# Optimization experiments

Hardware: AMD Instinct MI355X
Metric: run time of the kernel (lower is better)

Reference implementation:

```python
import jax, jax.numpy as jnp
import numpy as np

E = 2048   # embed_dim
H = 16     # num query heads
D = E // H # head_dim = 128
B = 2
S = 2048


def setup_inputs() -> dict:
    key = jax.random.key(0)
    ks = jax.random.split(key, 12)
    sc = 0.02
    return {
        "input": jax.random.normal(ks[0], (B, S, E), jnp.float32),
        "kv": jax.random.normal(ks[1], (B, S, E), jnp.float32),
        "Wq": jax.random.normal(ks[2], (E, E), jnp.float32) * sc,
        "bq": jnp.zeros((E,), jnp.float32),
        "Wk": jax.random.normal(ks[3], (D, E), jnp.float32) * sc,
        "bk": jnp.zeros((D,), jnp.float32),
        "Wv": jax.random.normal(ks[4], (D, E), jnp.float32) * sc,
        "bv": jnp.zeros((D,), jnp.float32),
        "Wo": jax.random.normal(ks[5], (E, E), jnp.float32) * sc,
        "bo": jnp.zeros((E,), jnp.float32),
        "expanding_context": 0,
    }


def reference(input, kv, Wq, bq, Wk, bk, Wv, bv, Wo, bo, expanding_context):
    b, s, _ = input.shape
    # projections (torch Linear: x @ W.T + b)
    q = (input @ Wq.T + bq).reshape(b, s, H, D).transpose(0, 2, 1, 3)  # [B,H,S,D]
    k = kv @ Wk.T + bk  # [B,S,D] single KV head
    v = kv @ Wv.T + bv  # [B,S,D]
    # scores with single KV head broadcast across query heads
    scores = jnp.einsum('bhsd,btd->bhst', q, k) / jnp.sqrt(jnp.float32(D))
    causal = jnp.triu(jnp.ones((s, s), bool), k=1)  # True above diagonal
    scores = jnp.where(causal[None, None], jnp.float32(-jnp.inf), scores)
    attn = jax.nn.softmax(scores, axis=-1)
    out = jnp.einsum('bhst,btd->bhsd', attn, v)  # [B,H,S,D]
    out = out.transpose(0, 2, 1, 3).reshape(b, s, E)
    return out @ Wo.T + bo
```

## Files before the change

### kernel.cpp

```cpp
#include <hip/hip_runtime.h>

#define B_  2
#define S_  2048
#define E_  2048
#define H_  16
#define D_  128
#define BS_ (B_*S_)

typedef __bf16 bf16_t;
typedef __bf16 bf16x8 __attribute__((ext_vector_type(8)));
typedef __bf16 bf16x4 __attribute__((ext_vector_type(4)));
typedef float  f32x4  __attribute__((ext_vector_type(4)));
typedef float  f32x16 __attribute__((ext_vector_type(16)));

#define QSCALE 0.1275174131003543f

__device__ __forceinline__ void gld16(const bf16_t* g, bf16_t* l) {
    __builtin_amdgcn_global_load_lds(
        (const __attribute__((address_space(1))) void*)g,
        (__attribute__((address_space(3))) void*)l,
        16, 0, 0);
}

__global__ void cvt_all(const float* __restrict__ s0, const float* __restrict__ s1,
                        const float* __restrict__ s2, const float* __restrict__ s3,
                        const float* __restrict__ s4, const float* __restrict__ s5,
                        bf16_t* d0, bf16_t* d1, bf16_t* d2,
                        bf16_t* d3, bf16_t* d4, bf16_t* d5)
{
    long i = ((long)blockIdx.x * blockDim.x + threadIdx.x) * 4;
    const float* s; bf16_t* d;
    if      (i <  8388608) { s = s0; d = d0; }
    else if (i < 16777216) { s = s1; d = d1; i -=  8388608; }
    else if (i < 20971520) { s = s2; d = d2; i -= 16777216; }
    else if (i < 21233664) { s = s3; d = d3; i -= 20971520; }
    else if (i < 21495808) { s = s4; d = d4; i -= 21233664; }
    else                   { s = s5; d = d5; i -= 21495808; }
    float4 v = *(const float4*)(s + i);
    bf16x4 o;
    o[0] = (bf16_t)v.x; o[1] = (bf16_t)v.y; o[2] = (bf16_t)v.z; o[3] = (bf16_t)v.w;
    *(bf16x4*)(d + i) = o;
}

template<int EP>
__device__ __forceinline__ void gemm_tile128(
    const bf16_t* __restrict__ A, const bf16_t* __restrict__ W,
    const float* __restrict__ bias,
    float* __restrict__ Cf, bf16_t* __restrict__ Cb,
    int N, int K, float scale, int m0, int w_n0, int c_n0,
    bf16_t* As, bf16_t* Bs)
{
    const int tid  = threadIdx.x;
    const int wave = tid >> 6, lane = tid & 63;
    const int wm = wave >> 1, wn = wave & 1;
    const int lrow = lane & 15, quad = lane >> 4;
    const int r8 = lane >> 3, c8 = (lane & 7) << 3;

    f32x4 acc[4][4] = {};

    for (int k0 = 0; k0 < K; k0 += 64) {
        __syncthreads();
#pragma unroll
        for (int j = 0; j < 4; ++j) {
            int base = (wave * 4 + j) * 8;
            gld16(A + (size_t)(m0 + base + r8) * K + k0 + c8, &As[base * 64]);
        }
#pragma unroll
        for (int j = 0; j < 4; ++j) {
            int base = (wave * 4 + j) * 8;
            gld16(W + (size_t)(w_n0 + base + r8) * K + k0 + c8, &Bs[base * 64]);
        }
        __syncthreads();
#pragma unroll
        for (int ks = 0; ks < 2; ++ks) {
            bf16x8 af[4], bfr[4];
#pragma unroll
            for (int mt = 0; mt < 4; ++mt)
                af[mt] = *(const bf16x8*)&As[(wm * 64 + mt * 16 + lrow) * 64 + ks * 32 + quad * 8];
#pragma unroll
            for (int nt = 0; nt < 4; ++nt)
                bfr[nt] = *(const bf16x8*)&Bs[(wn * 64 + nt * 16 + lrow) * 64 + ks * 32 + quad * 8];
#pragma unroll
            for (int mt = 0; mt < 4; ++mt)
#pragma unroll
                for (int nt = 0; nt < 4; ++nt)
                    acc[mt][nt] = __builtin_amdgcn_mfma_f32_16x16x32_bf16(
                        af[mt], bfr[nt], acc[mt][nt], 0, 0, 0);
        }
    }

#pragma unroll
    for (int mt = 0; mt < 4; ++mt) {
#pragma unroll
        for (int nt = 0; nt < 4; ++nt) {
            int lcol = wn * 64 + nt * 16 + lrow;
            int col = c_n0 + lcol;
            float bvv = bias[lcol];
#pragma unroll
            for (int r = 0; r < 4; ++r) {
                int row = m0 + wm * 64 + mt * 16 + quad * 4 + r;
                float v = (acc[mt][nt][r] + bvv) * scale;
                if (EP == 0) Cf[(size_t)row * N + col] = v;
                else         Cb[(size_t)row * N + col] = (bf16_t)v;
            }
        }
    }
}

__global__ __launch_bounds__(256) void gemm_qkv(
    const bf16_t* __restrict__ xb, const bf16_t* __restrict__ kvb,
    const bf16_t* __restrict__ Wq, const bf16_t* __restrict__ Wkv,
    const float* __restrict__ bq, const float* __restrict__ bk,
    const float* __restrict__ bv,
    bf16_t* __restrict__ Qb, bf16_t* __restrict__ KVb)
{
    __shared__ __align__(16) bf16_t As[128 * 64];
    __shared__ __align__(16) bf16_t Bs[128 * 64];
    const int m0 = blockIdx.y * 128;
    const int x = blockIdx.x;
    if (x < 16) {
        int n0 = x * 128;
        gemm_tile128<1>(xb, Wq, bq + n0, nullptr, Qb, E_, E_, QSCALE,
                        m0, n0, n0, As, Bs);
    } else if (x == 16) {
        gemm_tile128<1>(kvb, Wkv, bk, nullptr, KVb, 256, E_, 1.0f,
                        m0, 0, 0, As, Bs);
    } else {
        gemm_tile128<1>(kvb, Wkv, bv, nullptr, KVb, 256, E_, 1.0f,
                        m0, 128, 128, As, Bs);
    }
}

__global__ __launch_bounds__(256) void gemm_o(
    const bf16_t* __restrict__ A, const bf16_t* __restrict__ W,
    const float* __restrict__ bias, float* __restrict__ Cf)
{
    __shared__ __align__(16) bf16_t As[128 * 64];
    __shared__ __align__(16) bf16_t Bs[128 * 64];
    int n0 = blockIdx.x * 128;
    gemm_tile128<0>(A, W, bias + n0, Cf, nullptr, E_, E_, 1.0f,
                    blockIdx.y * 128, n0, n0, As, Bs);
}

__global__ __launch_bounds__(256, 2) void mqa_attn(
    const bf16_t* __restrict__ Q, const bf16_t* __restrict__ KV,
    bf16_t* __restrict__ O)
{
    __shared__ __align__(16) bf16_t Kt[2][64][136];
    __shared__ __align__(16) bf16_t Vt[2][128][72];

    const int bx = blockIdx.x, h = blockIdx.y, b = blockIdx.z;
    const int qb = b ? bx : (15 - bx);
    const int tid = threadIdx.x, wave = tid >> 6, lane = tid & 63;
    const int ln = lane & 31, hi = lane >> 5;
    const int q0w = qb * 128 + wave * 32;

    const bf16_t* kvp = KV + (size_t)(b * S_) * 256;

    bf16x8 qf[8];
    {
        const bf16_t* qp = Q + ((size_t)(b * S_ + q0w + ln)) * E_ + h * D_ + hi * 8;
#pragma unroll
        for (int st = 0; st < 8; ++st) qf[st] = *(const bf16x8*)(qp + st * 16);
    }

    bf16x8 ones;
#pragma unroll
    for (int j = 0; j < 8; ++j) ones[j] = (bf16_t)1.0f;

    f32x16 oacc[4] = {};
    f32x16 racc = {};
    bf16x8 af[4] = {};

    const int NT = 2 * qb + 2;
    const int Tw = (q0w + 31) >> 6;

    bf16x8 kreg[4], vA[2], vB[2];
    auto loadKV = [&](int kt) {
        const int k0 = kt * 64;
#pragma unroll
        for (int i = 0; i < 4; ++i) {
            int c = tid + 256 * i;
            kreg[i] = *(const bf16x8*)(kvp + (size_t)(k0 + (c >> 4)) * 256 + ((c & 15) << 3));
        }
#pragma unroll
        for (int i = 0; i < 2; ++i) {
            int c = tid + 256 * i;
            int n = (c & 31) * 2, d0 = (c >> 5) << 3;
            const bf16_t* src = kvp + (size_t)(k0 + n) * 256 + 128 + d0;
            vA[i] = *(const bf16x8*)src;
            vB[i] = *(const bf16x8*)(src + 256);
        }
    };
    auto stageWrite = [&](int bb) {
#pragma unroll
        for (int i = 0; i < 4; ++i) {
            int c = tid + 256 * i;
            *(bf16x8*)&Kt[bb][c >> 4][(c & 15) << 3] = kreg[i];
        }
#pragma unroll
        for (int i = 0; i < 2; ++i) {
            int c = tid + 256 * i;
            int n = (c & 31) * 2, d0 = (c >> 5) << 3;
#pragma unroll
            for (int j = 0; j < 8; ++j) {
                union { bf16_t h[2]; unsigned u; } w2;
                w2.h[0] = vA[i][j]; w2.h[1] = vB[i][j];
                *(unsigned*)&Vt[bb][d0 + j][n] = w2.u;
            }
        }
    };
    auto doPV = [&](int vb) {
        __builtin_amdgcn_s_setprio(1);
#pragma unroll
        for (int ks = 0; ks < 4; ++ks)
#pragma unroll
            for (int dt = 0; dt < 4; ++dt) {
                bf16x8 vf = *(const bf16x8*)&Vt[vb][dt * 32 + ln][ks * 16 + hi * 8];
                oacc[dt] = __builtin_amdgcn_mfma_f32_32x32x16_bf16(af[ks], vf, oacc[dt], 0, 0, 0);
            }
        __builtin_amdgcn_s_setprio(0);
    };

    loadKV(0);
    stageWrite(0);
    if (NT > 1) loadKV(1);

    for (int t = 0; t < NT; ++t) {
        const int cur = t & 1;
        if (t >= 1 && t - 1 <= Tw) doPV(cur ^ 1);
        __syncthreads();
        if (t + 1 < NT) stageWrite(cur ^ 1);
        if (t + 2 < NT) loadKV(t + 2);
        if (t <= Tw) {
            f32x16 sc[2] = {f32x16{}, f32x16{}};
            __builtin_amdgcn_s_setprio(1);
#pragma unroll
            for (int st = 0; st < 8; ++st) {
                bf16x8 qv = qf[st];
#pragma unroll
                for (int ct = 0; ct < 2; ++ct) {
                    bf16x8 kf = *(const bf16x8*)&Kt[cur][ct * 32 + ln][st * 16 + hi * 8];
                    sc[ct] = __builtin_amdgcn_mfma_f32_32x32x16_bf16(kf, qv, sc[ct], 0, 0, 0);
                }
            }
            __builtin_amdgcn_s_setprio(0);
            const int k_base = t * 64;
            const int qi = q0w + ln;
            if (k_base + 63 > q0w) {
#pragma unroll
                for (int ct = 0; ct < 2; ++ct)
#pragma unroll
                    for (int r = 0; r < 16; ++r) {
                        int kj = k_base + ct * 32 + (r & 3) + 8 * (r >> 2) + 4 * hi;
                        float s = (kj > qi) ? -1e30f : sc[ct][r];
                        sc[ct][r] = exp2f(s);
                    }
            } else {
#pragma unroll
                for (int ct = 0; ct < 2; ++ct)
#pragma unroll
                    for (int r = 0; r < 16; ++r)
                        sc[ct][r] = exp2f(sc[ct][r]);
            }
#pragma unroll
            for (int ks = 0; ks < 4; ++ks) {
                const int c = ks >> 1, b8 = (ks & 1) * 8;
                union { bf16_t h[2]; unsigned u; } pk0, pk1, pk2, pk3;
                pk0.h[0] = (bf16_t)sc[c][b8 + 0]; pk0.h[1] = (bf16_t)sc[c][b8 + 1];
                pk1.h[0] = (bf16_t)sc[c][b8 + 2]; pk1.h[1] = (bf16_t)sc[c][b8 + 3];
                pk2.h[0] = (bf16_t)sc[c][b8 + 4]; pk2.h[1] = (bf16_t)sc[c][b8 + 5];
                pk3.h[0] = (bf16_t)sc[c][b8 + 6]; pk3.h[1] = (bf16_t)sc[c][b8 + 7];
                const unsigned U0 = pk0.u, U1 = pk1.u, U2 = pk2.u, U3 = pk3.u;
                const unsigned V0 = __shfl_xor(U0, 32);
                const unsigned V1 = __shfl_xor(U1, 32);
                const unsigned V2 = __shfl_xor(U2, 32);
                const unsigned V3 = __shfl_xor(U3, 32);
                union { unsigned u[4]; bf16x8 v; } W;
                W.u[0] = hi ? V2 : U0;
                W.u[1] = hi ? V3 : U1;
                W.u[2] = hi ? U2 : V0;
                W.u[3] = hi ? U3 : V1;
                af[ks] = W.v;
            }
#pragma unroll
            for (int ks = 0; ks < 4; ++ks)
                racc = __builtin_amdgcn_mfma_f32_32x32x16_bf16(af[ks], ones, racc, 0, 0, 0);
        }
    }
    if (Tw == NT - 1) doPV(1);

    float inv[16];
#pragma unroll
    for (int r = 0; r < 16; ++r) inv[r] = 1.0f / racc[r];
#pragma unroll
    for (int dt = 0; dt < 4; ++dt)
#pragma unroll
        for (int r = 0; r < 16; ++r) {
            int ro = (r & 3) + 8 * (r >> 2) + 4 * hi;
            O[((size_t)(b * S_ + q0w + ro)) * E_ + h * D_ + dt * 32 + ln] =
                (bf16_t)(oacc[dt][r] * inv[r]);
        }
}

extern "C" void kernel_launch(void* const* d_in, const int* in_sizes, int n_in,
                              void* d_out, int out_size, void* d_ws, size_t ws_size,
                              hipStream_t stream)
{
    const float* x   = (const float*)d_in[0];
    const float* kv  = (const float*)d_in[1];
    const float* Wq  = (const float*)d_in[2];
    const float* bq  = (const float*)d_in[3];
    const float* Wk  = (const float*)d_in[4];
    const float* bk  = (const float*)d_in[5];
    const float* Wv  = (const float*)d_in[6];
    const float* bv  = (const float*)d_in[7];
    const float* Wo  = (const float*)d_in[8];
    const float* bo  = (const float*)d_in[9];
    float* out = (float*)d_out;

    bf16_t* p    = (bf16_t*)d_ws;
    bf16_t* xb   = p;  p += (size_t)BS_ * E_;
    bf16_t* kvb  = p;  p += (size_t)BS_ * E_;
    bf16_t* Wqb  = p;  p += (size_t)E_ * E_;
    bf16_t* Wkvb = p;  p += (size_t)2 * D_ * E_;
    bf16_t* Wob  = p;  p += (size_t)E_ * E_;
    bf16_t* Qb   = p;  p += (size_t)BS_ * E_;
    bf16_t* KVb  = p;  p += (size_t)BS_ * 256;
    bf16_t* Ob   = p;  p += (size_t)BS_ * E_;

    cvt_all<<<dim3(25088), dim3(256), 0, stream>>>(
        x, kv, Wq, Wk, Wv, Wo,
        xb, kvb, Wqb, Wkvb, Wkvb + (size_t)D_ * E_, Wob);

    gemm_qkv<<<dim3(18, BS_ / 128), 256, 0, stream>>>(
        xb, kvb, Wqb, Wkvb, bq, bk, bv, Qb, KVb);

    mqa_attn<<<dim3(S_ / 128, H_, B_), 256, 0, stream>>>(Qb, KVb, Ob);

    gemm_o<<<dim3(E_ / 128, BS_ / 128), 256, 0, stream>>>(Ob, Wob, bo, out);
}
```

Measured before the change: 357.4 us.

## Split-K the Q and output projections in two, merging partials downstream

The Q projection and the output projection now split the K dimension into two halves via a z grid dimension. Each half writes a bf16 partial buffer. The two Q partials are summed, biased and scaled while the attention kernel loads Q, and a new merge kernel adds the output partials plus bias into the fp32 result. The aim is more blocks per GEMM for better CU utilisation, at the cost of extra partial-buffer traffic, an extra kernel launch and bf16 rounding of the partial sums.

```diff
diff --git a/kernel.cpp b/kernel.cpp
--- a/kernel.cpp
+++ b/kernel.cpp
@@ -46,8 +46,8 @@
 __device__ __forceinline__ void gemm_tile128(
     const bf16_t* __restrict__ A, const bf16_t* __restrict__ W,
     const float* __restrict__ bias,
-    float* __restrict__ Cf, bf16_t* __restrict__ Cb,
-    int N, int K, float scale, int m0, int w_n0, int c_n0,
+    bf16_t* __restrict__ Cb,
+    int N, int K, int kb, int ke, float scale, int m0, int w_n0, int c_n0,
     bf16_t* As, bf16_t* Bs)
 {
     const int tid  = threadIdx.x;
@@ -58,7 +58,7 @@
 
     f32x4 acc[4][4] = {};
 
-    for (int k0 = 0; k0 < K; k0 += 64) {
+    for (int k0 = kb; k0 < ke; k0 += 64) {
         __syncthreads();
 #pragma unroll
         for (int j = 0; j < 4; ++j) {
@@ -95,13 +95,13 @@
         for (int nt = 0; nt < 4; ++nt) {
             int lcol = wn * 64 + nt * 16 + lrow;
             int col = c_n0 + lcol;
-            float bvv = bias[lcol];
+            float bvv = (EP == 1) ? bias[lcol] : 0.f;
 #pragma unroll
             for (int r = 0; r < 4; ++r) {
                 int row = m0 + wm * 64 + mt * 16 + quad * 4 + r;
-                float v = (acc[mt][nt][r] + bvv) * scale;
-                if (EP == 0) Cf[(size_t)row * N + col] = v;
-                else         Cb[(size_t)row * N + col] = (bf16_t)v;
+                float v = (EP == 1) ? (acc[mt][nt][r] + bvv) * scale
+                                    : acc[mt][nt][r];
+                Cb[(size_t)row * N + col] = (bf16_t)v;
             }
         }
     }
@@ -110,41 +110,62 @@
 __global__ __launch_bounds__(256) void gemm_qkv(
     const bf16_t* __restrict__ xb, const bf16_t* __restrict__ kvb,
     const bf16_t* __restrict__ Wq, const bf16_t* __restrict__ Wkv,
-    const float* __restrict__ bq, const float* __restrict__ bk,
-    const float* __restrict__ bv,
-    bf16_t* __restrict__ Qb, bf16_t* __restrict__ KVb)
+    const float* __restrict__ bk, const float* __restrict__ bv,
+    bf16_t* __restrict__ Qp0, bf16_t* __restrict__ Qp1,
+    bf16_t* __restrict__ KVb)
 {
     __shared__ __align__(16) bf16_t As[128 * 64];
     __shared__ __align__(16) bf16_t Bs[128 * 64];
     const int m0 = blockIdx.y * 128;
-    const int x = blockIdx.x;
+    const int x = blockIdx.x, z = blockIdx.z;
     if (x < 16) {
         int n0 = x * 128;
-        gemm_tile128<1>(xb, Wq, bq + n0, nullptr, Qb, E_, E_, QSCALE,
-                        m0, n0, n0, As, Bs);
-    } else if (x == 16) {
-        gemm_tile128<1>(kvb, Wkv, bk, nullptr, KVb, 256, E_, 1.0f,
-                        m0, 0, 0, As, Bs);
-    } else {
-        gemm_tile128<1>(kvb, Wkv, bv, nullptr, KVb, 256, E_, 1.0f,
-                        m0, 128, 128, As, Bs);
+        bf16_t* Qz = z ? Qp1 : Qp0;
+        gemm_tile128<2>(xb, Wq, nullptr, Qz, E_, E_,
+                        z * 1024, z * 1024 + 1024, 1.0f, m0, n0, n0, As, Bs);
+    } else if (z == 0) {
+        if (x == 16)
+            gemm_tile128<1>(kvb, Wkv, bk, KVb, 256, E_, 0, E_, 1.0f,
+                            m0, 0, 0, As, Bs);
+        else
+            gemm_tile128<1>(kvb, Wkv, bv, KVb, 256, E_, 0, E_, 1.0f,
+                            m0, 128, 128, As, Bs);
     }
 }
 
 __global__ __launch_bounds__(256) void gemm_o(
     const bf16_t* __restrict__ A, const bf16_t* __restrict__ W,
-    const float* __restrict__ bias, float* __restrict__ Cf)
+    bf16_t* __restrict__ Op0, bf16_t* __restrict__ Op1)
 {
     __shared__ __align__(16) bf16_t As[128 * 64];
     __shared__ __align__(16) bf16_t Bs[128 * 64];
-    int n0 = blockIdx.x * 128;
-    gemm_tile128<0>(A, W, bias + n0, Cf, nullptr, E_, E_, 1.0f,
+    const int n0 = blockIdx.x * 128, z = blockIdx.z;
+    bf16_t* Oz = z ? Op1 : Op0;
+    gemm_tile128<2>(A, W, nullptr, Oz, E_, E_,
+                    z * 1024, z * 1024 + 1024, 1.0f,
                     blockIdx.y * 128, n0, n0, As, Bs);
 }
 
+__global__ __launch_bounds__(256) void merge_out(
+    const bf16_t* __restrict__ p0, const bf16_t* __restrict__ p1,
+    const float* __restrict__ bo, float* __restrict__ out)
+{
+    long i = ((long)blockIdx.x * blockDim.x + threadIdx.x) * 4;
+    bf16x4 a = *(const bf16x4*)(p0 + i);
+    bf16x4 b = *(const bf16x4*)(p1 + i);
+    float4 bb = *(const float4*)(bo + (i & 2047));
+    float4 o;
+    o.x = (float)a[0] + (float)b[0] + bb.x;
+    o.y = (float)a[1] + (float)b[1] + bb.y;
+    o.z = (float)a[2] + (float)b[2] + bb.z;
+    o.w = (float)a[3] + (float)b[3] + bb.w;
+    *(float4*)(out + i) = o;
+}
+
 __global__ __launch_bounds__(256, 2) void mqa_attn(
-    const bf16_t* __restrict__ Q, const bf16_t* __restrict__ KV,
-    bf16_t* __restrict__ O)
+    const bf16_t* __restrict__ Qp0, const bf16_t* __restrict__ Qp1,
+    const float* __restrict__ bq,
+    const bf16_t* __restrict__ KV, bf16_t* __restrict__ O)
 {
     __shared__ __align__(16) bf16_t Kt[2][64][136];
     __shared__ __align__(16) bf16_t Vt[2][128][72];
@@ -159,9 +180,24 @@
 
     bf16x8 qf[8];
     {
-        const bf16_t* qp = Q + ((size_t)(b * S_ + q0w + ln)) * E_ + h * D_ + hi * 8;
-#pragma unroll
-        for (int st = 0; st < 8; ++st) qf[st] = *(const bf16x8*)(qp + st * 16);
+        size_t off = ((size_t)(b * S_ + q0w + ln)) * E_ + h * D_ + hi * 8;
+        const bf16_t* q0p = Qp0 + off;
+        const bf16_t* q1p = Qp1 + off;
+        const float* bqp = bq + h * D_ + hi * 8;
+#pragma unroll
+        for (int st = 0; st < 8; ++st) {
+            bf16x8 a0 = *(const bf16x8*)(q0p + st * 16);
+            bf16x8 a1 = *(const bf16x8*)(q1p + st * 16);
+            float4 c0 = *(const float4*)(bqp + st * 16);
+            float4 c1 = *(const float4*)(bqp + st * 16 + 4);
+            const float* cb0 = (const float*)&c0;
+            const float* cb1 = (const float*)&c1;
+#pragma unroll
+            for (int j = 0; j < 8; ++j) {
+                float bb = (j < 4) ? cb0[j] : cb1[j - 4];
+                qf[st][j] = (bf16_t)(((float)a0[j] + (float)a1[j] + bb) * QSCALE);
+            }
+        }
     }
 
     bf16x8 ones;
@@ -325,18 +361,21 @@
     bf16_t* Wqb  = p;  p += (size_t)E_ * E_;
     bf16_t* Wkvb = p;  p += (size_t)2 * D_ * E_;
     bf16_t* Wob  = p;  p += (size_t)E_ * E_;
-    bf16_t* Qb   = p;  p += (size_t)BS_ * E_;
+    bf16_t* Qp0  = p;  p += (size_t)BS_ * E_;
     bf16_t* KVb  = p;  p += (size_t)BS_ * 256;
     bf16_t* Ob   = p;  p += (size_t)BS_ * E_;
+    bf16_t* Qp1  = p;  p += (size_t)BS_ * E_;
 
     cvt_all<<<dim3(25088), dim3(256), 0, stream>>>(
         x, kv, Wq, Wk, Wv, Wo,
         xb, kvb, Wqb, Wkvb, Wkvb + (size_t)D_ * E_, Wob);
 
-    gemm_qkv<<<dim3(18, BS_ / 128), 256, 0, stream>>>(
-        xb, kvb, Wqb, Wkvb, bq, bk, bv, Qb, KVb);
-
-    mqa_attn<<<dim3(S_ / 128, H_, B_), 256, 0, stream>>>(Qb, KVb, Ob);
-
-    gemm_o<<<dim3(E_ / 128, BS_ / 128), 256, 0, stream>>>(Ob, Wob, bo, out);
-}
+    gemm_qkv<<<dim3(18, BS_ / 128, 2), 256, 0, stream>>>(
+        xb, kvb, Wqb, Wkvb, bk, bv, Qp0, Qp1, KVb);
+
+    mqa_attn<<<dim3(S_ / 128, H_, B_), 256, 0, stream>>>(Qp0, Qp1, bq, KVb, Ob);
+
+    gemm_o<<<dim3(E_ / 128, BS_ / 128, 2), 256, 0, stream>>>(Ob, Wob, xb, kvb);
+
+    merge_out<<<dim3(8192), dim3(256), 0, stream>>>(xb, kvb, bo, out);
+}
```

Result: no change. 352.6 us (-1.4%).
